# Performance work log

Hardware: AMD Instinct MI355X
Metric: run time of the kernel (lower is better)

Reference implementation:

```python
import jax, jax.numpy as jnp
import numpy as np


def setup_inputs() -> dict:
    key = jax.random.key(0)
    k1, k2, k3 = jax.random.split(key, 3)
    x = jax.random.normal(k1, (32, 256, 64, 64), dtype=jnp.float32)
    w = jax.random.normal(k2, (1, 1, 7, 7), dtype=jnp.float32) * (1.0 / 7.0)
    b = jax.random.normal(k3, (1,), dtype=jnp.float32) * 0.1
    return {"x": x, "w": w, "b": b}


def reference(x, w, b):
    # channel-wise mean and max pooling, keepdim -> [B,1,H,W]
    pooled = jnp.mean(x, axis=1, keepdims=True) + jnp.max(x, axis=1, keepdims=True)
    # 7x7 conv, 1->1 channel, SAME padding (pad=3)
    attn = jax.lax.conv_general_dilated(
        pooled, w,
        window_strides=(1, 1),
        padding=((3, 3), (3, 3)),
        dimension_numbers=("NCHW", "OIHW", "NCHW"),
    ) + b[None, :, None, None]
    attn = jax.nn.sigmoid(attn)
    return x * attn  # broadcast over channels
```

## Files before the change

### kernel.cpp

```cpp
#include <hip/hip_runtime.h>
#include <math.h>

#define BATCH 32
#define CH    256
#define HH    64
#define WW    64
#define HW    (HH * WW)
#define NPIX  (BATCH * HW)
#define PG    (NPIX / 4)
#define NTOT  ((size_t)BATCH * CH * HW)
#define NCHUNK 8
#define CCHUNK (CH / NCHUNK)

typedef float floatx4 __attribute__((ext_vector_type(4)));

__global__ __launch_bounds__(256) void sa_pool_partial_kernel(
    const float* __restrict__ x,
    float4* __restrict__ pSum, float4* __restrict__ pMax) {
    int t = blockIdx.x * blockDim.x + threadIdx.x;
    int pg    = t & (PG - 1);
    int chunk = t >> 15;
    int b   = pg >> 10;
    int hwg = pg & 1023;
    const float4* p = reinterpret_cast<const float4*>(
        x + (size_t)b * CH * HW + (size_t)chunk * CCHUNK * HW) + hwg;
    float4 s = make_float4(0.f, 0.f, 0.f, 0.f);
    float4 m = make_float4(-INFINITY, -INFINITY, -INFINITY, -INFINITY);
#pragma unroll 8
    for (int c = 0; c < CCHUNK; ++c) {
        float4 v = p[c * (HW / 4)];
        s.x += v.x; s.y += v.y; s.z += v.z; s.w += v.w;
        m.x = fmaxf(m.x, v.x); m.y = fmaxf(m.y, v.y);
        m.z = fmaxf(m.z, v.z); m.w = fmaxf(m.w, v.w);
    }
    pSum[chunk * PG + pg] = s;
    pMax[chunk * PG + pg] = m;
}

__global__ __launch_bounds__(256) void sa_pool_combine_kernel(
    const float4* __restrict__ pSum, const float4* __restrict__ pMax,
    float4* __restrict__ pooled) {
    int pg = blockIdx.x * blockDim.x + threadIdx.x;
    if (pg >= PG) return;
    float4 s = make_float4(0.f, 0.f, 0.f, 0.f);
    float4 m = make_float4(-INFINITY, -INFINITY, -INFINITY, -INFINITY);
#pragma unroll
    for (int c = 0; c < NCHUNK; ++c) {
        float4 sv = pSum[c * PG + pg];
        float4 mv = pMax[c * PG + pg];
        s.x += sv.x; s.y += sv.y; s.z += sv.z; s.w += sv.w;
        m.x = fmaxf(m.x, mv.x); m.y = fmaxf(m.y, mv.y);
        m.z = fmaxf(m.z, mv.z); m.w = fmaxf(m.w, mv.w);
    }
    const float inv = 1.0f / (float)CH;
    float4 o;
    o.x = s.x * inv + m.x; o.y = s.y * inv + m.y;
    o.z = s.z * inv + m.z; o.w = s.w * inv + m.w;
    pooled[pg] = o;
}

__global__ __launch_bounds__(256) void sa_conv_kernel(
    const float* __restrict__ pooled, const float* __restrict__ wgt,
    const float* __restrict__ bias, float* __restrict__ attn) {
    int idx = blockIdx.x * blockDim.x + threadIdx.x;
    if (idx >= NPIX) return;
    int b  = idx >> 12;
    int hw = idx & 4095;
    int h  = hw >> 6;
    int w  = hw & 63;
    const float* pb = pooled + b * HW;
    float acc = bias[0];
#pragma unroll
    for (int kh = 0; kh < 7; ++kh) {
        int hh2 = h + kh - 3;
        if (hh2 < 0 || hh2 >= HH) continue;
#pragma unroll
        for (int kw = 0; kw < 7; ++kw) {
            int ww2 = w + kw - 3;
            if (ww2 < 0 || ww2 >= WW) continue;
            acc += pb[hh2 * WW + ww2] * wgt[kh * 7 + kw];
        }
    }
    attn[idx] = 1.0f / (1.0f + __expf(-acc));
}

__global__ __launch_bounds__(256) void sa_mul_kernel(
    const float* __restrict__ x, const float* __restrict__ attn,
    float* __restrict__ out) {
    size_t i = ((size_t)blockIdx.x * blockDim.x + threadIdx.x) * 4;
    if (i >= NTOT) return;
    size_t bc = i >> 12;
    int hw    = (int)(i & 4095);
    int b     = (int)(bc >> 8);
    float4 xv = *reinterpret_cast<const float4*>(x + i);
    float4 av = *reinterpret_cast<const float4*>(attn + (size_t)b * HW + hw);
    floatx4 o;
    o.x = xv.x * av.x;
    o.y = xv.y * av.y;
    o.z = xv.z * av.z;
    o.w = xv.w * av.w;
    __builtin_nontemporal_store(o, reinterpret_cast<floatx4*>(out + i));
}

extern "C" void kernel_launch(void* const* d_in, const int* in_sizes, int n_in,
                              void* d_out, int out_size, void* d_ws, size_t ws_size,
                              hipStream_t stream) {
    const float* x    = (const float*)d_in[0];
    const float* wgt  = (const float*)d_in[1];
    const float* bias = (const float*)d_in[2];
    float* out = (float*)d_out;

    float*  pooled = (float*)d_ws;
    float*  attn   = pooled + NPIX;
    float4* pSum   = reinterpret_cast<float4*>(attn + NPIX);
    float4* pMax   = pSum + (size_t)NCHUNK * PG;

    {
        dim3 block(256);
        dim3 grid((PG * NCHUNK) / 256);
        sa_pool_partial_kernel<<<grid, block, 0, stream>>>(x, pSum, pMax);
    }
    {
        dim3 block(256);
        dim3 grid((PG + 255) / 256);
        sa_pool_combine_kernel<<<grid, block, 0, stream>>>(
            pSum, pMax, reinterpret_cast<float4*>(pooled));
    }
    {
        dim3 block(256);
        dim3 grid((NPIX + 255) / 256);
        sa_conv_kernel<<<grid, block, 0, stream>>>(pooled, wgt, bias, attn);
    }
    {
        dim3 block(256);
        dim3 grid((unsigned)((NTOT / 4 + 255) / 256));
        sa_mul_kernel<<<grid, block, 0, stream>>>(x, attn, out);
    }
}
```

Baseline: 78.64 us.

## Fuse pool-combine with 7x7 conv and loop channels in multiply kernel

Merges the partial-sum combine and the 7x7 convolution into one kernel. Each block combines a 16-row band plus halo of the pooled map into shared memory and convolves it there, which drops one launch and the global round trip for the pooled map. The channel split is halved from 8 to 4 chunks. The multiply kernel now loads attn once per thread and loops over 64 channels. Fewer threads are launched for the two bandwidth-heavy passes, which may lower occupancy and memory-level parallelism.

```diff
diff --git a/kernel.cpp b/kernel.cpp
--- a/kernel.cpp
+++ b/kernel.cpp
@@ -9,15 +9,15 @@
 #define NPIX  (BATCH * HW)
 #define PG    (NPIX / 4)
 #define NTOT  ((size_t)BATCH * CH * HW)
-#define NCHUNK 8
+#define NCHUNK 4
 #define CCHUNK (CH / NCHUNK)
 
 typedef float floatx4 __attribute__((ext_vector_type(4)));
 
-__global__ __launch_bounds__(256) void sa_pool_partial_kernel(
+__global__ __launch_bounds__(256) void sa_pool_partial(
     const float* __restrict__ x,
     float4* __restrict__ pSum, float4* __restrict__ pMax) {
-    int t = blockIdx.x * blockDim.x + threadIdx.x;
+    int t = blockIdx.x * 256 + threadIdx.x;
     int pg    = t & (PG - 1);
     int chunk = t >> 15;
     int b   = pg >> 10;
@@ -37,69 +37,81 @@
     pMax[chunk * PG + pg] = m;
 }
 
-__global__ __launch_bounds__(256) void sa_pool_combine_kernel(
+__global__ __launch_bounds__(256) void sa_comb_conv(
     const float4* __restrict__ pSum, const float4* __restrict__ pMax,
-    float4* __restrict__ pooled) {
-    int pg = blockIdx.x * blockDim.x + threadIdx.x;
-    if (pg >= PG) return;
-    float4 s = make_float4(0.f, 0.f, 0.f, 0.f);
-    float4 m = make_float4(-INFINITY, -INFINITY, -INFINITY, -INFINITY);
+    const float* __restrict__ wgt, const float* __restrict__ bias,
+    float* __restrict__ attn) {
+    __shared__ float pooled[22][64];
+    __shared__ float wq[49];
+    int bidx = blockIdx.x;
+    int b = bidx >> 2;
+    int s = bidx & 3;
+    int t = threadIdx.x;
+    if (t < 49) wq[t] = wgt[t];
+    int rowbase = 16 * s - 3; if (rowbase < 0) rowbase = 0;
+    int rowend  = 16 * s + 19; if (rowend > 64) rowend = 64;
+    int nrows   = rowend - rowbase;
+    int ngroups = nrows * 16;
+    const float inv = 1.0f / (float)CH;
+    for (int i = t; i < ngroups; i += 256) {
+        int lr = i >> 4, cg = i & 15;
+        int pg = b * 1024 + (rowbase + lr) * 16 + cg;
+        float4 sv = make_float4(0.f, 0.f, 0.f, 0.f);
+        float4 mv = make_float4(-INFINITY, -INFINITY, -INFINITY, -INFINITY);
 #pragma unroll
-    for (int c = 0; c < NCHUNK; ++c) {
-        float4 sv = pSum[c * PG + pg];
-        float4 mv = pMax[c * PG + pg];
-        s.x += sv.x; s.y += sv.y; s.z += sv.z; s.w += sv.w;
-        m.x = fmaxf(m.x, mv.x); m.y = fmaxf(m.y, mv.y);
-        m.z = fmaxf(m.z, mv.z); m.w = fmaxf(m.w, mv.w);
+        for (int c = 0; c < NCHUNK; ++c) {
+            float4 a  = pSum[c * PG + pg];
+            float4 bm = pMax[c * PG + pg];
+            sv.x += a.x; sv.y += a.y; sv.z += a.z; sv.w += a.w;
+            mv.x = fmaxf(mv.x, bm.x); mv.y = fmaxf(mv.y, bm.y);
+            mv.z = fmaxf(mv.z, bm.z); mv.w = fmaxf(mv.w, bm.w);
+        }
+        pooled[lr][cg * 4 + 0] = sv.x * inv + mv.x;
+        pooled[lr][cg * 4 + 1] = sv.y * inv + mv.y;
+        pooled[lr][cg * 4 + 2] = sv.z * inv + mv.z;
+        pooled[lr][cg * 4 + 3] = sv.w * inv + mv.w;
     }
-    const float inv = 1.0f / (float)CH;
-    float4 o;
-    o.x = s.x * inv + m.x; o.y = s.y * inv + m.y;
-    o.z = s.z * inv + m.z; o.w = s.w * inv + m.w;
-    pooled[pg] = o;
+    __syncthreads();
+    float bv = bias[0];
+    for (int i = t; i < 1024; i += 256) {
+        int r = i >> 6, w = i & 63;
+        int gr = 16 * s + r;
+        float acc = bv;
+#pragma unroll
+        for (int kh = 0; kh < 7; ++kh) {
+            int gr2 = gr + kh - 3;
+            if (gr2 < 0 || gr2 >= HH) continue;
+            int lr = gr2 - rowbase;
+#pragma unroll
+            for (int kw = 0; kw < 7; ++kw) {
+                int w2 = w + kw - 3;
+                if (w2 < 0 || w2 >= WW) continue;
+                acc += pooled[lr][w2] * wq[kh * 7 + kw];
+            }
+        }
+        attn[b * HW + gr * 64 + w] = 1.0f / (1.0f + __expf(-acc));
+    }
 }
 
-__global__ __launch_bounds__(256) void sa_conv_kernel(
-    const float* __restrict__ pooled, const float* __restrict__ wgt,
-    const float* __restrict__ bias, float* __restrict__ attn) {
-    int idx = blockIdx.x * blockDim.x + threadIdx.x;
-    if (idx >= NPIX) return;
-    int b  = idx >> 12;
-    int hw = idx & 4095;
-    int h  = hw >> 6;
-    int w  = hw & 63;
-    const float* pb = pooled + b * HW;
-    float acc = bias[0];
-#pragma unroll
-    for (int kh = 0; kh < 7; ++kh) {
-        int hh2 = h + kh - 3;
-        if (hh2 < 0 || hh2 >= HH) continue;
-#pragma unroll
-        for (int kw = 0; kw < 7; ++kw) {
-            int ww2 = w + kw - 3;
-            if (ww2 < 0 || ww2 >= WW) continue;
-            acc += pb[hh2 * WW + ww2] * wgt[kh * 7 + kw];
-        }
+__global__ __launch_bounds__(256) void sa_mul(
+    const float* __restrict__ x, const float4* __restrict__ attn4,
+    float* __restrict__ out) {
+    int t = blockIdx.x * 256 + threadIdx.x;
+    int pg = t & (PG - 1);
+    int cq = t >> 15;
+    int b  = pg >> 10;
+    float4 a = attn4[pg];
+    size_t base = (size_t)b * CH * HW + (size_t)cq * CCHUNK * HW
+                + (size_t)(pg & 1023) * 4;
+    const float* xp = x + base;
+    float* op = out + base;
+#pragma unroll 8
+    for (int c = 0; c < CCHUNK; ++c) {
+        float4 v = *reinterpret_cast<const float4*>(xp + (size_t)c * HW);
+        floatx4 o;
+        o.x = v.x * a.x; o.y = v.y * a.y; o.z = v.z * a.z; o.w = v.w * a.w;
+        __builtin_nontemporal_store(o, reinterpret_cast<floatx4*>(op + (size_t)c * HW));
     }
-    attn[idx] = 1.0f / (1.0f + __expf(-acc));
-}
-
-__global__ __launch_bounds__(256) void sa_mul_kernel(
-    const float* __restrict__ x, const float* __restrict__ attn,
-    float* __restrict__ out) {
-    size_t i = ((size_t)blockIdx.x * blockDim.x + threadIdx.x) * 4;
-    if (i >= NTOT) return;
-    size_t bc = i >> 12;
-    int hw    = (int)(i & 4095);
-    int b     = (int)(bc >> 8);
-    float4 xv = *reinterpret_cast<const float4*>(x + i);
-    float4 av = *reinterpret_cast<const float4*>(attn + (size_t)b * HW + hw);
-    floatx4 o;
-    o.x = xv.x * av.x;
-    o.y = xv.y * av.y;
-    o.z = xv.z * av.z;
-    o.w = xv.w * av.w;
-    __builtin_nontemporal_store(o, reinterpret_cast<floatx4*>(out + i));
 }
 
 extern "C" void kernel_launch(void* const* d_in, const int* in_sizes, int n_in,
@@ -110,30 +122,14 @@
     const float* bias = (const float*)d_in[2];
     float* out = (float*)d_out;
 
-    float*  pooled = (float*)d_ws;
-    float*  attn   = pooled + NPIX;
-    float4* pSum   = reinterpret_cast<float4*>(attn + NPIX);
-    float4* pMax   = pSum + (size_t)NCHUNK * PG;
+    float*  attn = (float*)d_ws;
+    float4* pSum = reinterpret_cast<float4*>(attn + NPIX);
+    float4* pMax = pSum + (size_t)NCHUNK * PG;
 
-    {
-        dim3 block(256);
-        dim3 grid((PG * NCHUNK) / 256);
-        sa_pool_partial_kernel<<<grid, block, 0, stream>>>(x, pSum, pMax);
-    }
-    {
-        dim3 block(256);
-        dim3 grid((PG + 255) / 256);
-        sa_pool_combine_kernel<<<grid, block, 0, stream>>>(
-            pSum, pMax, reinterpret_cast<float4*>(pooled));
-    }
-    {
-        dim3 block(256);
-        dim3 grid((NPIX + 255) / 256);
-        sa_conv_kernel<<<grid, block, 0, stream>>>(pooled, wgt, bias, attn);
-    }
-    {
-        dim3 block(256);
-        dim3 grid((unsigned)((NTOT / 4 + 255) / 256));
-        sa_mul_kernel<<<grid, block, 0, stream>>>(x, attn, out);
-    }
+    sa_pool_partial<<<dim3((PG * NCHUNK) / 256), dim3(256), 0, stream>>>(
+        x, pSum, pMax);
+    sa_comb_conv<<<dim3(BATCH * 4), dim3(256), 0, stream>>>(
+        pSum, pMax, wgt, bias, attn);
+    sa_mul<<<dim3((PG * NCHUNK) / 256), dim3(256), 0, stream>>>(
+        x, reinterpret_cast<const float4*>(attn), out);
 }
```

Result: slower. 82.87 us (+5.4%).
